# Kernel optimization log

Measured on AMD Instinct MI355X. Metric: run time of the kernel, lower is better.

The kernel has to match this reference:

```python
import jax, jax.numpy as jnp
import numpy as np

B, T, D = 8, 512, 64

def setup_inputs() -> dict:
    key = jax.random.key(0)
    kx, kw, kb = jax.random.split(key, 3)
    x = jax.random.normal(kx, (B, T, D), dtype=jnp.float32)
    W = jax.random.normal(kw, (D, D), dtype=jnp.float32) / np.sqrt(D)
    b = jax.random.normal(kb, (D,), dtype=jnp.float32) * 0.01
    return {"x": x, "W": W, "b": b}

def reference(x, W, b):
    # v = Linear(x): (B,T,D)
    v = jnp.einsum('btd,ed->bte', x, W) + b
    # pairwise diff: (B,T,T,D); softmax over feature dim D
    diff = x[:, :, None, :] - x[:, None, :, :]
    K = jax.nn.softmax(-(diff * diff), axis=-1)
    # out[b,i,j] = sum_d K[b,i,j,d] * v[b,i,d]  -> (B,T,T)
    out = jnp.einsum('bijd,bid->bij', K, v)
    return out
```

## Files before the change

kernel.cpp:

```cpp
#include <hip/hip_runtime.h>

#define BB 8
#define TT 512
#define DD 64
#define IT 4
#define JT 64
#define LDP 65

__device__ __forceinline__ float fast_exp2(float v) {
#if __has_builtin(__builtin_amdgcn_exp2f)
    return __builtin_amdgcn_exp2f(v);
#else
    return exp2f(v);
#endif
}

__global__ __launch_bounds__(256) void rbf_fused2(
    const float* __restrict__ x,
    const float* __restrict__ W,
    const float* __restrict__ bias,
    float* __restrict__ out)
{
    const int blk = blockIdx.x;
    const int b   = blk >> 7;
    const int i0  = (blk & 127) * IT;
    const int t   = threadIdx.x;
    const int w   = t >> 6;
    const int l   = t & 63;

    __shared__ float xi_s[IT][DD];
    __shared__ float vi_s[IT][DD];
    __shared__ float xj_s[JT][LDP];

    const float S = 1.2011224087864498f;

    const float* xrow = x + (size_t)(b * TT + i0 + w) * DD;
    {
        const float* wrow = W + (size_t)l * DD;
        float acc = bias[l];
        #pragma unroll
        for (int d = 0; d < DD; d += 4) {
            float4 xv = *reinterpret_cast<const float4*>(xrow + d);
            float4 wv = *reinterpret_cast<const float4*>(wrow + d);
            acc = fmaf(xv.x, wv.x, acc);
            acc = fmaf(xv.y, wv.y, acc);
            acc = fmaf(xv.z, wv.z, acc);
            acc = fmaf(xv.w, wv.w, acc);
        }
        vi_s[w][l] = acc;
        xi_s[w][l] = xrow[l] * S;
    }
    __syncthreads();

    float4 xi_r[16];
    #pragma unroll
    for (int c = 0; c < 16; ++c)
        xi_r[c] = *reinterpret_cast<const float4*>(&xi_s[w][c * 4]);

    const float* xb   = x + (size_t)b * TT * DD;
    float*       orow = out + (size_t)(b * TT + i0 + w) * TT;

    for (int jt = 0; jt < TT / JT; ++jt) {
        if (jt) __syncthreads();
        #pragma unroll
        for (int u = 0; u < 4; ++u) {
            int idx = u * 256 + t;
            int r = idx >> 4;
            int c = (idx & 15) * 4;
            float4 v = *reinterpret_cast<const float4*>(
                xb + (size_t)(jt * JT + r) * DD + c);
            xj_s[r][c + 0] = v.x * S;
            xj_s[r][c + 1] = v.y * S;
            xj_s[r][c + 2] = v.z * S;
            xj_s[r][c + 3] = v.w * S;
        }
        __syncthreads();

        float num = 0.f, den = 0.f;
        #pragma unroll
        for (int c = 0; c < 16; ++c) {
            float4 xj = *reinterpret_cast<const float4*>(&xj_s[l][c * 4]);
            float4 vi = *reinterpret_cast<const float4*>(&vi_s[w][c * 4]);
            float4 xi = xi_r[c];
            float d0 = xi.x - xj.x;
            float d1 = xi.y - xj.y;
            float d2 = xi.z - xj.z;
            float d3 = xi.w - xj.w;
            float e0 = fast_exp2(-(d0 * d0));
            float e1 = fast_exp2(-(d1 * d1));
            float e2 = fast_exp2(-(d2 * d2));
            float e3 = fast_exp2(-(d3 * d3));
            num = fmaf(e0, vi.x, num);
            num = fmaf(e1, vi.y, num);
            num = fmaf(e2, vi.z, num);
            num = fmaf(e3, vi.w, num);
            den += (e0 + e1) + (e2 + e3);
        }
        orow[jt * JT + l] = num / den;
    }
}

extern "C" void kernel_launch(void* const* d_in, const int* in_sizes, int n_in,
                              void* d_out, int out_size, void* d_ws, size_t ws_size,
                              hipStream_t stream) {
    const float* x    = (const float*)d_in[0];
    const float* W    = (const float*)d_in[1];
    const float* bias = (const float*)d_in[2];
    float* out        = (float*)d_out;

    rbf_fused2<<<BB * (TT / IT), 256, 0, stream>>>(x, W, bias, out);
}
```

Baseline: 93.87 us.

## Double-buffer j-tiles, split j across two blocks, scalarize xi broadcast

The grid doubles, and each block now covers half of the j range, which adds parallelism. The j tile for the next step is prefetched into registers and written into a double-buffered shared array, padded to 17 float4 per row. This overlaps global loads with exp compute and needs only one barrier per tile. Because xi is uniform across the wave, it is broadcast through readfirstlane into scalar registers, vi is kept in registers, and the division is replaced with a fast reciprocal. The cost is that each block recomputes the vi projection twice, register pressure rises under the 4-wave occupancy hint, and the approximate reciprocal adds slight precision risk.

```diff
diff --git a/kernel.cpp b/kernel.cpp
--- a/kernel.cpp
+++ b/kernel.cpp
@@ -4,8 +4,10 @@
 #define TT 512
 #define DD 64
 #define IT 4
-#define JT 64
-#define LDP 65
+#define JTILE 64
+#define NTILE 4
+#define GR 17
+#define S_SCALE 1.2011224087864498f
 
 __device__ __forceinline__ float fast_exp2(float v) {
 #if __has_builtin(__builtin_amdgcn_exp2f)
@@ -14,78 +16,103 @@
     return exp2f(v);
 #endif
 }
+__device__ __forceinline__ float fast_rcp(float v) {
+#if __has_builtin(__builtin_amdgcn_rcpf)
+    return __builtin_amdgcn_rcpf(v);
+#else
+    return 1.0f / v;
+#endif
+}
+__device__ __forceinline__ float bcast0(float v) {
+    return __int_as_float(__builtin_amdgcn_readfirstlane(__float_as_int(v)));
+}
 
-__global__ __launch_bounds__(256) void rbf_fused2(
+__global__ __launch_bounds__(256, 4) void rbf_fused3(
     const float* __restrict__ x,
     const float* __restrict__ W,
     const float* __restrict__ bias,
     float* __restrict__ out)
 {
     const int blk = blockIdx.x;
-    const int b   = blk >> 7;
-    const int i0  = (blk & 127) * IT;
+    const int jh  = blk & 1;
+    const int it  = (blk >> 1) & 127;
+    const int b   = blk >> 8;
     const int t   = threadIdx.x;
     const int w   = t >> 6;
     const int l   = t & 63;
 
     __shared__ float xi_s[IT][DD];
     __shared__ float vi_s[IT][DD];
-    __shared__ float xj_s[JT][LDP];
+    __shared__ float xj_s[2][JTILE * GR * 4];
 
-    const float S = 1.2011224087864498f;
-
-    const float* xrow = x + (size_t)(b * TT + i0 + w) * DD;
+    const float* xrow = x + (size_t)(b * TT + it * IT + w) * DD;
     {
-        const float* wrow = W + (size_t)l * DD;
+        const float* wr = W + (size_t)l * DD;
         float acc = bias[l];
         #pragma unroll
         for (int d = 0; d < DD; d += 4) {
-            float4 xv = *reinterpret_cast<const float4*>(xrow + d);
-            float4 wv = *reinterpret_cast<const float4*>(wrow + d);
-            acc = fmaf(xv.x, wv.x, acc);
-            acc = fmaf(xv.y, wv.y, acc);
-            acc = fmaf(xv.z, wv.z, acc);
-            acc = fmaf(xv.w, wv.w, acc);
+            float4 xv = *(const float4*)(xrow + d);
+            float4 wv = *(const float4*)(wr + d);
+            acc = fmaf(xv.x, wv.x, acc); acc = fmaf(xv.y, wv.y, acc);
+            acc = fmaf(xv.z, wv.z, acc); acc = fmaf(xv.w, wv.w, acc);
         }
         vi_s[w][l] = acc;
-        xi_s[w][l] = xrow[l] * S;
+        xi_s[w][l] = xrow[l] * S_SCALE;
     }
     __syncthreads();
 
-    float4 xi_r[16];
+    float4 vi_r[16];
+    float  sxi[DD];
     #pragma unroll
-    for (int c = 0; c < 16; ++c)
-        xi_r[c] = *reinterpret_cast<const float4*>(&xi_s[w][c * 4]);
+    for (int c = 0; c < 16; ++c) {
+        vi_r[c] = *(const float4*)(&vi_s[w][c * 4]);
+        float4 xv = *(const float4*)(&xi_s[w][c * 4]);
+        sxi[c * 4 + 0] = bcast0(xv.x);
+        sxi[c * 4 + 1] = bcast0(xv.y);
+        sxi[c * 4 + 2] = bcast0(xv.z);
+        sxi[c * 4 + 3] = bcast0(xv.w);
+    }
 
-    const float* xb   = x + (size_t)b * TT * DD;
-    float*       orow = out + (size_t)(b * TT + i0 + w) * TT;
+    const float* xb = x + ((size_t)b * TT + (size_t)jh * 256) * DD;
+    float* orow = out + (size_t)(b * TT + it * IT + w) * TT + jh * 256;
 
-    for (int jt = 0; jt < TT / JT; ++jt) {
-        if (jt) __syncthreads();
+    const int sr = t >> 4;
+    const int sc = t & 15;
+    float4 pf[4];
+
+    #pragma unroll
+    for (int u = 0; u < 4; ++u)
+        pf[u] = *(const float4*)(xb + (size_t)(u * 16 + sr) * DD + sc * 4);
+    {
+        float4* dst = (float4*)xj_s[0];
         #pragma unroll
         for (int u = 0; u < 4; ++u) {
-            int idx = u * 256 + t;
-            int r = idx >> 4;
-            int c = (idx & 15) * 4;
-            float4 v = *reinterpret_cast<const float4*>(
-                xb + (size_t)(jt * JT + r) * DD + c);
-            xj_s[r][c + 0] = v.x * S;
-            xj_s[r][c + 1] = v.y * S;
-            xj_s[r][c + 2] = v.z * S;
-            xj_s[r][c + 3] = v.w * S;
+            float4 v = pf[u];
+            v.x *= S_SCALE; v.y *= S_SCALE; v.z *= S_SCALE; v.w *= S_SCALE;
+            dst[(u * 16 + sr) * GR + sc] = v;
         }
-        __syncthreads();
+    }
+    __syncthreads();
 
+    int buf = 0;
+    for (int jt = 0; jt < NTILE; ++jt) {
+        if (jt + 1 < NTILE) {
+            #pragma unroll
+            for (int u = 0; u < 4; ++u)
+                pf[u] = *(const float4*)(
+                    xb + (size_t)((jt + 1) * JTILE + u * 16 + sr) * DD + sc * 4);
+        }
+
+        const float4* xjs = (const float4*)xj_s[buf];
         float num = 0.f, den = 0.f;
         #pragma unroll
-        for (int c = 0; c < 16; ++c) {
-            float4 xj = *reinterpret_cast<const float4*>(&xj_s[l][c * 4]);
-            float4 vi = *reinterpret_cast<const float4*>(&vi_s[w][c * 4]);
-            float4 xi = xi_r[c];
-            float d0 = xi.x - xj.x;
-            float d1 = xi.y - xj.y;
-            float d2 = xi.z - xj.z;
-            float d3 = xi.w - xj.w;
+        for (int cc = 0; cc < 16; ++cc) {
+            float4 xj = xjs[l * GR + cc];
+            float4 vi = vi_r[cc];
+            float d0 = sxi[cc * 4 + 0] - xj.x;
+            float d1 = sxi[cc * 4 + 1] - xj.y;
+            float d2 = sxi[cc * 4 + 2] - xj.z;
+            float d3 = sxi[cc * 4 + 3] - xj.w;
             float e0 = fast_exp2(-(d0 * d0));
             float e1 = fast_exp2(-(d1 * d1));
             float e2 = fast_exp2(-(d2 * d2));
@@ -96,7 +123,19 @@
             num = fmaf(e3, vi.w, num);
             den += (e0 + e1) + (e2 + e3);
         }
-        orow[jt * JT + l] = num / den;
+        orow[jt * JTILE + l] = num * fast_rcp(den);
+
+        if (jt + 1 < NTILE) {
+            float4* dst = (float4*)xj_s[buf ^ 1];
+            #pragma unroll
+            for (int u = 0; u < 4; ++u) {
+                float4 v = pf[u];
+                v.x *= S_SCALE; v.y *= S_SCALE; v.z *= S_SCALE; v.w *= S_SCALE;
+                dst[(u * 16 + sr) * GR + sc] = v;
+            }
+            __syncthreads();
+            buf ^= 1;
+        }
     }
 }
 
@@ -108,5 +147,5 @@
     const float* bias = (const float*)d_in[2];
     float* out        = (float*)d_out;
 
-    rbf_fused2<<<BB * (TT / IT), 256, 0, stream>>>(x, W, bias, out);
+    rbf_fused3<<<BB * (TT / IT) * 2, 256, 0, stream>>>(x, W, bias, out);
 }
```

Result: faster. 91.36 us (-2.7%).

## Exploit pairwise symmetry to compute both out[i,j] and out[j,i] from shared exponentials

Applied to the files above, without the earlier changes.

Splits the work into a precompute kernel (linear projection and scaled x to workspace) and a pair kernel that visits only lower-triangular tile pairs. Because the squared difference and softmax denominator are symmetric in i and j, each exponential serves both out[i,j] and out[j,i], roughly halving the transcendental work. Transposed results are staged in shared memory for coalesced writes, and the division is replaced with a hardware reciprocal. It adds a second launch, a workspace round-trip and an uneven block-index decode.

```diff
diff --git a/kernel.cpp b/kernel.cpp
--- a/kernel.cpp
+++ b/kernel.cpp
@@ -3,9 +3,7 @@
 #define BB 8
 #define TT 512
 #define DD 64
-#define IT 4
-#define JT 64
-#define LDP 65
+#define S_SCALE 1.2011224087864498f
 
 __device__ __forceinline__ float fast_exp2(float v) {
 #if __has_builtin(__builtin_amdgcn_exp2f)
@@ -14,89 +12,120 @@
     return exp2f(v);
 #endif
 }
+__device__ __forceinline__ float fast_rcp(float v) {
+#if __has_builtin(__builtin_amdgcn_rcpf)
+    return __builtin_amdgcn_rcpf(v);
+#else
+    return 1.0f / v;
+#endif
+}
 
-__global__ __launch_bounds__(256) void rbf_fused2(
-    const float* __restrict__ x,
-    const float* __restrict__ W,
-    const float* __restrict__ bias,
+__global__ __launch_bounds__(256) void rbf_pre(
+    const float* __restrict__ x, const float* __restrict__ W,
+    const float* __restrict__ bias, float* __restrict__ xsc,
+    float* __restrict__ vv)
+{
+    const int t = threadIdx.x;
+    const int w = t >> 6, l = t & 63;
+    const int row = blockIdx.x * 4 + w;
+    const float* xr = x + (size_t)row * DD;
+    const float* wr = W + (size_t)l * DD;
+    float acc = bias[l];
+    #pragma unroll
+    for (int d = 0; d < DD; d += 4) {
+        float4 xv = *(const float4*)(xr + d);
+        float4 wv = *(const float4*)(wr + d);
+        acc = fmaf(xv.x, wv.x, acc); acc = fmaf(xv.y, wv.y, acc);
+        acc = fmaf(xv.z, wv.z, acc); acc = fmaf(xv.w, wv.w, acc);
+    }
+    vv [(size_t)row * DD + l] = acc;
+    xsc[(size_t)row * DD + l] = xr[l] * S_SCALE;
+}
+
+__global__ __launch_bounds__(256, 3) void rbf_pair(
+    const float* __restrict__ xsc, const float* __restrict__ vv,
     float* __restrict__ out)
 {
-    const int blk = blockIdx.x;
-    const int b   = blk >> 7;
-    const int i0  = (blk & 127) * IT;
-    const int t   = threadIdx.x;
-    const int w   = t >> 6;
-    const int l   = t & 63;
+    const int bid = blockIdx.x;
+    const int b   = bid / 144;
+    const int idx = bid - b * 144;
+    int st, jt, isA;
+    if (idx < 32) { jt = idx >> 2; st = 4 * jt + (idx & 3); isA = 0; }
+    else {
+        int k = idx - 32, tt = 1;
+        while (k >= 4 * tt) { k -= 4 * tt; ++tt; }
+        jt = tt; st = k; isA = 1;
+    }
+    const int tid = threadIdx.x;
+    const int w = __builtin_amdgcn_readfirstlane(tid >> 6);
+    const int l = tid & 63;
 
-    __shared__ float xi_s[IT][DD];
-    __shared__ float vi_s[IT][DD];
-    __shared__ float xj_s[JT][LDP];
+    __shared__ float xls[64 * 68];
+    __shared__ float vls[64 * 68];
+    __shared__ float cbuf[64 * 20];
 
-    const float S = 1.2011224087864498f;
-
-    const float* xrow = x + (size_t)(b * TT + i0 + w) * DD;
-    {
-        const float* wrow = W + (size_t)l * DD;
-        float acc = bias[l];
-        #pragma unroll
-        for (int d = 0; d < DD; d += 4) {
-            float4 xv = *reinterpret_cast<const float4*>(xrow + d);
-            float4 wv = *reinterpret_cast<const float4*>(wrow + d);
-            acc = fmaf(xv.x, wv.x, acc);
-            acc = fmaf(xv.y, wv.y, acc);
-            acc = fmaf(xv.z, wv.z, acc);
-            acc = fmaf(xv.w, wv.w, acc);
-        }
-        vi_s[w][l] = acc;
-        xi_s[w][l] = xrow[l] * S;
+    const size_t jbase = ((size_t)b * TT + (size_t)jt * 64) * DD;
+    #pragma unroll
+    for (int u = 0; u < 4; ++u) {
+        int gg = u * 256 + tid;
+        int r = gg >> 4, c = gg & 15;
+        float4 a  = *(const float4*)(xsc + jbase + (size_t)r * DD + c * 4);
+        float4 vq = *(const float4*)(vv  + jbase + (size_t)r * DD + c * 4);
+        *(float4*)(&xls[r * 68 + c * 4]) = a;
+        *(float4*)(&vls[r * 68 + c * 4]) = vq;
     }
     __syncthreads();
 
-    float4 xi_r[16];
+    float4 xj_r[16];
     #pragma unroll
     for (int c = 0; c < 16; ++c)
-        xi_r[c] = *reinterpret_cast<const float4*>(&xi_s[w][c * 4]);
+        xj_r[c] = *(const float4*)(&xls[l * 68 + c * 4]);
 
-    const float* xb   = x + (size_t)b * TT * DD;
-    float*       orow = out + (size_t)(b * TT + i0 + w) * TT;
+    const int i0 = st * 16;
+    float* outb = out + (size_t)b * TT * TT;
 
-    for (int jt = 0; jt < TT / JT; ++jt) {
-        if (jt) __syncthreads();
-        #pragma unroll
-        for (int u = 0; u < 4; ++u) {
-            int idx = u * 256 + t;
-            int r = idx >> 4;
-            int c = (idx & 15) * 4;
-            float4 v = *reinterpret_cast<const float4*>(
-                xb + (size_t)(jt * JT + r) * DD + c);
-            xj_s[r][c + 0] = v.x * S;
-            xj_s[r][c + 1] = v.y * S;
-            xj_s[r][c + 2] = v.z * S;
-            xj_s[r][c + 3] = v.w * S;
-        }
-        __syncthreads();
-
-        float num = 0.f, den = 0.f;
+    #pragma unroll 1
+    for (int r = 0; r < 4; ++r) {
+        const int iloc = w * 4 + r;
+        const int irow = i0 + iloc;
+        const float4* xi4 = (const float4*)(xsc + ((size_t)b * TT + irow) * DD);
+        const float4* vi4 = (const float4*)(vv  + ((size_t)b * TT + irow) * DD);
+        float nr0 = 0.f, nr1 = 0.f, nc0 = 0.f, nc1 = 0.f, dn0 = 0.f, dn1 = 0.f;
         #pragma unroll
         for (int c = 0; c < 16; ++c) {
-            float4 xj = *reinterpret_cast<const float4*>(&xj_s[l][c * 4]);
-            float4 vi = *reinterpret_cast<const float4*>(&vi_s[w][c * 4]);
-            float4 xi = xi_r[c];
-            float d0 = xi.x - xj.x;
-            float d1 = xi.y - xj.y;
-            float d2 = xi.z - xj.z;
-            float d3 = xi.w - xj.w;
-            float e0 = fast_exp2(-(d0 * d0));
-            float e1 = fast_exp2(-(d1 * d1));
-            float e2 = fast_exp2(-(d2 * d2));
-            float e3 = fast_exp2(-(d3 * d3));
-            num = fmaf(e0, vi.x, num);
-            num = fmaf(e1, vi.y, num);
-            num = fmaf(e2, vi.z, num);
-            num = fmaf(e3, vi.w, num);
-            den += (e0 + e1) + (e2 + e3);
+            float4 xa = xi4[c];
+            float4 va = vi4[c];
+            float4 xj = xj_r[c];
+            float4 vj = *(const float4*)(&vls[l * 68 + c * 4]);
+            float u0 = xa.x - xj.x;
+            float u1 = xa.y - xj.y;
+            float u2 = xa.z - xj.z;
+            float u3 = xa.w - xj.w;
+            float e0 = fast_exp2(-(u0 * u0));
+            float e1 = fast_exp2(-(u1 * u1));
+            float e2 = fast_exp2(-(u2 * u2));
+            float e3 = fast_exp2(-(u3 * u3));
+            nr0 = fmaf(e0, va.x, nr0);
+            nr1 = fmaf(e1, va.y, nr1);
+            nr0 = fmaf(e2, va.z, nr0);
+            nr1 = fmaf(e3, va.w, nr1);
+            nc0 = fmaf(e0, vj.x, nc0);
+            nc1 = fmaf(e1, vj.y, nc1);
+            nc0 = fmaf(e2, vj.z, nc0);
+            nc1 = fmaf(e3, vj.w, nc1);
+            dn0 += e0 + e1;
+            dn1 += e2 + e3;
         }
-        orow[jt * JT + l] = num / den;
+        float rd = fast_rcp(dn0 + dn1);
+        outb[(size_t)irow * TT + jt * 64 + l] = (nr0 + nr1) * rd;
+        if (isA) cbuf[l * 20 + iloc] = (nc0 + nc1) * rd;
+    }
+
+    __syncthreads();
+    if (isA) {
+        int j = tid >> 2, q = tid & 3;
+        float4 cv = *(const float4*)(&cbuf[j * 20 + q * 4]);
+        *(float4*)(outb + ((size_t)jt * 64 + j) * TT + i0 + q * 4) = cv;
     }
 }
 
@@ -108,5 +137,9 @@
     const float* bias = (const float*)d_in[2];
     float* out        = (float*)d_out;
 
-    rbf_fused2<<<BB * (TT / IT), 256, 0, stream>>>(x, W, bias, out);
+    float* xsc = (float*)d_ws;
+    float* vv  = (float*)((char*)d_ws + (1 << 20));
+
+    rbf_pre <<<BB * TT / 4, 256, 0, stream>>>(x, W, bias, xsc, vv);
+    rbf_pair<<<BB * 144,     256, 0, stream>>>(xsc, vv, out);
 }
```

Measured after the change: 114.1 us. 1.22x slower.
